# Kernel tuning notes

Measured on AMD Instinct MI355X. Metric: run time of the kernel, lower is better.

Reference implementation:

```python
import jax, jax.numpy as jnp
import numpy as np

B, C, T = 64, 64, 1000   # batch, EEG channels (input_dim), timesteps
H = 512                   # hidden_dim
L = 3                     # num_layers
NC = 5                    # num_classes


def setup_inputs() -> dict:
    key = jax.random.key(0)
    ks = jax.random.split(key, 9)
    s_in = 1.0 / np.sqrt(H)  # torch LSTM init scale
    x = jax.random.normal(ks[0], (B, C, T), dtype=jnp.float32)
    W_ih0 = jax.random.uniform(ks[1], (4 * H, C), jnp.float32, -s_in, s_in)
    W_ih_rest = jax.random.uniform(ks[2], (L - 1, 4 * H, H), jnp.float32, -s_in, s_in)
    W_hh = jax.random.uniform(ks[3], (L, 4 * H, H), jnp.float32, -s_in, s_in)
    b_ih = jax.random.uniform(ks[4], (L, 4 * H), jnp.float32, -s_in, s_in)
    b_hh = jax.random.uniform(ks[5], (L, 4 * H), jnp.float32, -s_in, s_in)
    W_fc = jax.random.uniform(ks[6], (NC, H), jnp.float32, -s_in, s_in)
    b_fc = jax.random.uniform(ks[7], (NC,), jnp.float32, -s_in, s_in)
    return {"x": x, "W_ih0": W_ih0, "W_ih_rest": W_ih_rest, "W_hh": W_hh,
            "b_ih": b_ih, "b_hh": b_hh, "W_fc": W_fc, "b_fc": b_fc}


def _lstm_layer(x_tbc, W_ih, W_hh, b):
    """x_tbc: [T, B, in]. Returns (h_seq [T,B,H], h_T [B,H]). Gate order i,f,g,o (PyTorch)."""
    # Precompute input projections for all timesteps: [T, B, 4H]
    xg = jnp.einsum('tbi,gi->tbg', x_tbc, W_ih) + b

    def step(carry, xg_t):
        h, c = carry
        gates = xg_t + h @ W_hh.T  # [B, 4H]
        i, f, g, o = jnp.split(gates, 4, axis=-1)
        i, f, o = jax.nn.sigmoid(i), jax.nn.sigmoid(f), jax.nn.sigmoid(o)
        g = jnp.tanh(g)
        c = f * c + i * g
        h = o * jnp.tanh(c)
        return (h, c), h

    Bn = x_tbc.shape[1]
    h0 = jnp.zeros((Bn, H), x_tbc.dtype)
    (hT, _), h_seq = jax.lax.scan(step, (h0, h0), xg)
    return h_seq, hT


def reference(x, W_ih0, W_ih_rest, W_hh, b_ih, b_hh, W_fc, b_fc):
    # input_type='signal': [B, C, T] -> batch_first [B, T, C]; scan over time-major [T, B, C]
    seq = jnp.transpose(x, (2, 0, 1))  # [T, B, C]
    hT = None
    for l in range(L):
        W_ih = W_ih0 if l == 0 else W_ih_rest[l - 1]
        seq, hT = _lstm_layer(seq, W_ih, W_hh[l], b_ih[l] + b_hh[l])
    # dropout=0 (inference): identity
    return hT @ W_fc.T + b_fc  # [B, NC]
```

## Files before the change

kernel.cpp:

```cpp
#include <hip/hip_runtime.h>
#include <cstdint>

#define TB 64
#define TC 64
#define TT 1000
#define TH 512
#define NCLS 5
#define NTHR 512
#define STEPS 1002

#define H0_OFF 0
#define H1_OFF 8192
#define H2_OFF 16384
#define X_OFF  24576
#define SC_OFF 32768
#define SC_W   864
#define LDS_FLOATS (SC_OFF + 8 * SC_W)
#define LDS_BYTES  (LDS_FLOATS * 4)

__device__ __forceinline__ float sigf(float x) { return 1.0f / (1.0f + expf(-x)); }

__device__ __forceinline__ void pin4(float4& v) {
  asm volatile("" : "+v"(v.x), "+v"(v.y), "+v"(v.z), "+v"(v.w));
}

__device__ __forceinline__ void group_barrier(int* gb, int s) {
  __syncthreads();
  if (threadIdx.x == 0) {
    const int target = s + 1;
    int a = __hip_atomic_fetch_add(gb + 0, 1, __ATOMIC_RELAXED, __HIP_MEMORY_SCOPE_AGENT);
    if (a == 64 * target - 1)
      __hip_atomic_fetch_add(gb + 8, 1, __ATOMIC_RELAXED, __HIP_MEMORY_SCOPE_AGENT);
    while (__hip_atomic_load(gb + 8, __ATOMIC_RELAXED, __HIP_MEMORY_SCOPE_AGENT) < target)
      __builtin_amdgcn_s_sleep(1);
    unsigned xcc;
    asm volatile("s_getreg_b32 %0, hwreg(HW_REG_XCC_ID)" : "=s"(xcc));
    int expected = s;
    if (__hip_atomic_compare_exchange_strong(gb + 32 + (xcc & 7), &expected, target,
            __ATOMIC_RELAXED, __ATOMIC_RELAXED, __HIP_MEMORY_SCOPE_AGENT)) {
      __threadfence();
    }
    int d = __hip_atomic_fetch_add(gb + 16, 1, __ATOMIC_RELAXED, __HIP_MEMORY_SCOPE_AGENT);
    if (d == 64 * target - 1)
      __hip_atomic_fetch_add(gb + 24, 1, __ATOMIC_RELAXED, __HIP_MEMORY_SCOPE_AGENT);
    while (__hip_atomic_load(gb + 24, __ATOMIC_RELAXED, __HIP_MEMORY_SCOPE_AGENT) < target)
      __builtin_amdgcn_s_sleep(1);
  }
  __syncthreads();
}

__device__ __forceinline__ void dot4(float& acc, const float4 a, const float4 b) {
  acc = fmaf(a.x, b.x, acc); acc = fmaf(a.y, b.y, acc);
  acc = fmaf(a.z, b.z, acc); acc = fmaf(a.w, b.w, acc);
}

__device__ __forceinline__ void gload_lds16_cg(const char* gsrc_lane, char* lds_base) {
  __builtin_amdgcn_global_load_lds(
      (const __attribute__((address_space(1))) unsigned int*)gsrc_lane,
      (__attribute__((address_space(3))) unsigned int*)lds_base, 16, 0, 0x11);
}

__global__ __launch_bounds__(NTHR) __attribute__((amdgpu_waves_per_eu(2, 2)))
void lstm_pipe(
    const float* __restrict__ x, const float* __restrict__ Wih0,
    const float* __restrict__ WihR, const float* __restrict__ Whh,
    const float* __restrict__ bih, const float* __restrict__ bhh,
    float* __restrict__ hbuf, int* __restrict__ bar)
{
  __shared__ float lds[LDS_FLOATS];
  const int tid = threadIdx.x;
  const int blk = blockIdx.x;
  const int grp = blk >> 6, slot = blk & 63;
  const int b_base = grp * 16;
  const int kk = tid >> 5;
  const int rt = tid & 31;
  const int g  = rt & 3;
  const int cl = rt >> 2;
  const int cell = slot * 8 + cl;
  const int row  = g * TH + cell;
  const int wv = tid >> 6;
  const int lane = tid & 63;

  int* gb = bar + grp * 64;

  float4 wx, wh0[8], w1a[8], w1b[8], w2a[8], w2b[8];
  wx = *(const float4*)(Wih0 + (size_t)row * TC + 4 * kk);
  pin4(wx);
  {
    const float* p0 = Whh  + (size_t)row * TH + 32 * kk;
    const float* p1 = WihR + (size_t)row * TH + 32 * kk;
    const float* p2 = Whh  + (size_t)(2048 + row) * TH + 32 * kk;
    const float* p3 = WihR + (size_t)(2048 + row) * TH + 32 * kk;
    const float* p4 = Whh  + (size_t)(4096 + row) * TH + 32 * kk;
#pragma unroll
    for (int i = 0; i < 8; ++i) {
      wh0[i] = *(const float4*)(p0 + 4 * i); pin4(wh0[i]);
      w1a[i] = *(const float4*)(p1 + 4 * i); pin4(w1a[i]);
      w1b[i] = *(const float4*)(p2 + 4 * i); pin4(w1b[i]);
      w2a[i] = *(const float4*)(p3 + 4 * i); pin4(w2a[i]);
      w2b[i] = *(const float4*)(p4 + 4 * i); pin4(w2b[i]);
    }
  }

  const int rl = tid >> 6;
  const int rc = (tid & 63) >> 3;
  const int rb = tid & 7;
  const int rcell = slot * 8 + rc;
  float4 bias_r = make_float4(0.f, 0.f, 0.f, 0.f);
  if (tid < 192) {
    bias_r.x = bih[rl * 2048 + rcell]        + bhh[rl * 2048 + rcell];
    bias_r.y = bih[rl * 2048 +  512 + rcell] + bhh[rl * 2048 +  512 + rcell];
    bias_r.z = bih[rl * 2048 + 1024 + rcell] + bhh[rl * 2048 + 1024 + rcell];
    bias_r.w = bih[rl * 2048 + 1536 + rcell] + bhh[rl * 2048 + 1536 + rcell];
  }
  float cst0 = 0.f, cst1 = 0.f;

  for (int s = 0; s < STEPS; ++s) {
    {
      const bool v0 = (s >= 1 && s <= 1000);
      const bool v1 = (s >= 2);
      const bool v2 = (s >= 3);
      const bool vc = ((s & 7) == 0 && s <= 999);
      if (v0) {
        const char* gp = (const char*)(hbuf + ((size_t)(0 + ((s - 1) & 1)) * TB + b_base) * TH);
        char* lb = (char*)lds + H0_OFF * 4;
#pragma unroll
        for (int i = 0; i < 4; ++i) {
          int off = wv * 4096 + i * 1024;
          gload_lds16_cg(gp + off + lane * 16, lb + off);
        }
      }
      if (v1) {
        const char* gp = (const char*)(hbuf + ((size_t)(2 + ((s - 2) & 1)) * TB + b_base) * TH);
        char* lb = (char*)lds + H1_OFF * 4;
#pragma unroll
        for (int i = 0; i < 4; ++i) {
          int off = wv * 4096 + i * 1024;
          gload_lds16_cg(gp + off + lane * 16, lb + off);
        }
      }
      if (v2) {
        const char* gp = (const char*)(hbuf + ((size_t)(4 + ((s - 3) & 1)) * TB + b_base) * TH);
        char* lb = (char*)lds + H2_OFF * 4;
#pragma unroll
        for (int i = 0; i < 4; ++i) {
          int off = wv * 4096 + i * 1024;
          gload_lds16_cg(gp + off + lane * 16, lb + off);
        }
      }
      if (vc) {
        const int e0 = tid, e1 = tid + NTHR;
        const float* q0 = x + (size_t)(b_base + (e0 >> 6)) * (TC * TT) + (size_t)(e0 & 63) * TT + s;
        const float* q1 = x + (size_t)(b_base + (e1 >> 6)) * (TC * TT) + (size_t)(e1 & 63) * TT + s;
        float4 xa0 = *(const float4*)(q0), xa1 = *(const float4*)(q0 + 4);
        float4 xb0 = *(const float4*)(q1), xb1 = *(const float4*)(q1 + 4);
        float* d0 = lds + X_OFF + (e0 >> 6) * 64 + (e0 & 63);
        float* d1 = lds + X_OFF + (e1 >> 6) * 64 + (e1 & 63);
        d0[0 * 1024] = xa0.x; d0[1 * 1024] = xa0.y; d0[2 * 1024] = xa0.z; d0[3 * 1024] = xa0.w;
        d0[4 * 1024] = xa1.x; d0[5 * 1024] = xa1.y; d0[6 * 1024] = xa1.z; d0[7 * 1024] = xa1.w;
        d1[0 * 1024] = xb0.x; d1[1 * 1024] = xb0.y; d1[2 * 1024] = xb0.z; d1[3 * 1024] = xb0.w;
        d1[4 * 1024] = xb1.x; d1[5 * 1024] = xb1.y; d1[6 * 1024] = xb1.z; d1[7 * 1024] = xb1.w;
      }
    }
    __syncthreads();

#pragma unroll
    for (int p = 0; p < 2; ++p) {
      float a0[8], a1[8], a2[8];
#pragma unroll
      for (int b = 0; b < 8; ++b) { a0[b] = 0.f; a1[b] = 0.f; a2[b] = 0.f; }
#pragma unroll
      for (int b = 0; b < 8; ++b) {
        const int bb = p * 8 + b;
        if (s <= 999) {
          float4 xf = *(const float4*)(lds + X_OFF + (s & 7) * 1024 + bb * 64 + 4 * kk);
          dot4(a0[b], wx, xf);
        }
        if (s >= 1 && s <= 1000) {
          const float* hb = lds + H0_OFF + bb * TH + 32 * kk;
#pragma unroll
          for (int c4 = 0; c4 < 2; ++c4) {
            float4 f0 = *(const float4*)(hb + 16 * c4 + 0);
            float4 f1 = *(const float4*)(hb + 16 * c4 + 4);
            float4 f2 = *(const float4*)(hb + 16 * c4 + 8);
            float4 f3 = *(const float4*)(hb + 16 * c4 + 12);
            if (s <= 999) {
              dot4(a0[b], wh0[4 * c4 + 0], f0); dot4(a0[b], wh0[4 * c4 + 1], f1);
              dot4(a0[b], wh0[4 * c4 + 2], f2); dot4(a0[b], wh0[4 * c4 + 3], f3);
            }
            dot4(a1[b], w1a[4 * c4 + 0], f0); dot4(a1[b], w1a[4 * c4 + 1], f1);
            dot4(a1[b], w1a[4 * c4 + 2], f2); dot4(a1[b], w1a[4 * c4 + 3], f3);
          }
        }
        if (s >= 2) {
          const float* hb = lds + H1_OFF + bb * TH + 32 * kk;
#pragma unroll
          for (int c4 = 0; c4 < 2; ++c4) {
            float4 f0 = *(const float4*)(hb + 16 * c4 + 0);
            float4 f1 = *(const float4*)(hb + 16 * c4 + 4);
            float4 f2 = *(const float4*)(hb + 16 * c4 + 8);
            float4 f3 = *(const float4*)(hb + 16 * c4 + 12);
            if (s <= 1000) {
              dot4(a1[b], w1b[4 * c4 + 0], f0); dot4(a1[b], w1b[4 * c4 + 1], f1);
              dot4(a1[b], w1b[4 * c4 + 2], f2); dot4(a1[b], w1b[4 * c4 + 3], f3);
            }
            dot4(a2[b], w2a[4 * c4 + 0], f0); dot4(a2[b], w2a[4 * c4 + 1], f1);
            dot4(a2[b], w2a[4 * c4 + 2], f2); dot4(a2[b], w2a[4 * c4 + 3], f3);
          }
        }
        if (s >= 3) {
          const float* hb = lds + H2_OFF + bb * TH + 32 * kk;
#pragma unroll
          for (int c4 = 0; c4 < 2; ++c4) {
            float4 f0 = *(const float4*)(hb + 16 * c4 + 0);
            float4 f1 = *(const float4*)(hb + 16 * c4 + 4);
            float4 f2 = *(const float4*)(hb + 16 * c4 + 8);
            float4 f3 = *(const float4*)(hb + 16 * c4 + 12);
            dot4(a2[b], w2b[4 * c4 + 0], f0); dot4(a2[b], w2b[4 * c4 + 1], f1);
            dot4(a2[b], w2b[4 * c4 + 2], f2); dot4(a2[b], w2b[4 * c4 + 3], f3);
          }
        }
      }
#pragma unroll
      for (int b = 0; b < 8; ++b) {
        a0[b] += __shfl_xor(a0[b], 32, 64);
        a1[b] += __shfl_xor(a1[b], 32, 64);
        a2[b] += __shfl_xor(a2[b], 32, 64);
      }
      if ((tid & 32) == 0) {
        float* sb = lds + SC_OFF + wv * SC_W + cl * 36 + g;
#pragma unroll
        for (int b = 0; b < 8; ++b) {
          sb[4 * b]       = a0[b];
          sb[288 + 4 * b] = a1[b];
          sb[576 + 4 * b] = a2[b];
        }
      }
      __syncthreads();
      if (tid < 192) {
        const int tl = s - rl;
        if (tl >= 0 && tl < TT) {
          float sx = 0.f, sy = 0.f, sz = 0.f, sw = 0.f;
          const float* sb = lds + SC_OFF + rl * 288 + rc * 36 + 4 * rb;
#pragma unroll
          for (int w8 = 0; w8 < 8; ++w8) {
            float4 v = *(const float4*)(sb + w8 * SC_W);
            sx += v.x; sy += v.y; sz += v.z; sw += v.w;
          }
          float ii = sigf(sx + bias_r.x);
          float ff = sigf(sy + bias_r.y);
          float gg = tanhf(sz + bias_r.z);
          float oo = sigf(sw + bias_r.w);
          float cprev = p ? cst1 : cst0;
          float cc = (tl == 0) ? ii * gg : fmaf(ff, cprev, ii * gg);
          if (p) cst1 = cc; else cst0 = cc;
          float hh = oo * tanhf(cc);
          hbuf[((size_t)(rl * 2 + (tl & 1)) * TB + b_base + p * 8 + rb) * TH + rcell] = hh;
        }
      }
      __syncthreads();
    }
    group_barrier(gb, s);
  }
}

__global__ void fc_kernel(const float* __restrict__ hbuf, const float* __restrict__ Wfc,
                          const float* __restrict__ bfc, float* __restrict__ out) {
  int bb = blockIdx.x, lane = threadIdx.x;
  const float* h = hbuf + ((size_t)5 * TB + bb) * TH;
  for (int n = 0; n < NCLS; ++n) {
    float s = 0.f;
    for (int k = lane; k < TH; k += 64) s = fmaf(h[k], Wfc[n * TH + k], s);
    for (int off = 32; off > 0; off >>= 1) s += __shfl_down(s, off, 64);
    if (lane == 0) out[bb * NCLS + n] = s + bfc[n];
  }
}

extern "C" void kernel_launch(void* const* d_in, const int* in_sizes, int n_in,
                              void* d_out, int out_size, void* d_ws, size_t ws_size,
                              hipStream_t stream) {
  const float* x    = (const float*)d_in[0];
  const float* Wih0 = (const float*)d_in[1];
  const float* WihR = (const float*)d_in[2];
  const float* Whh  = (const float*)d_in[3];
  const float* bih  = (const float*)d_in[4];
  const float* bhh  = (const float*)d_in[5];
  const float* Wfc  = (const float*)d_in[6];
  const float* bfc  = (const float*)d_in[7];
  float* out = (float*)d_out;

  char* ws = (char*)d_ws;
  int*   bar  = (int*)ws;
  float* hbuf = (float*)(ws + 1024);

  hipMemsetAsync(bar, 0, 1024, stream);
  lstm_pipe<<<256, NTHR, 0, stream>>>(x, Wih0, WihR, Whh, bih, bhh, hbuf, bar);
  fc_kernel<<<TB, 64, 0, stream>>>(hbuf, Wfc, bfc, out);
}
```

Baseline: 18.64 ms.

## Replace two-phase grid barrier with hierarchical per-XCD barrier

The grid barrier used by every timestep becomes hierarchical. At startup each block counts how many blocks share its XCD and how many XCDs are occupied. Each step, blocks increment a per-XCD counter, and only the last block on each XCD fences and bumps a global counter. All blocks then spin on a single release flag. This cuts contended global atomics and removes one full spin phase per step. The risk is memory-ordering correctness, since only one fence is issued per XCD.

```diff
diff --git a/kernel.cpp b/kernel.cpp
--- a/kernel.cpp
+++ b/kernel.cpp
@@ -24,26 +24,19 @@
   asm volatile("" : "+v"(v.x), "+v"(v.y), "+v"(v.z), "+v"(v.w));
 }
 
-__device__ __forceinline__ void group_barrier(int* gb, int s) {
+__device__ __forceinline__ void group_barrier(int* gb, int s, unsigned xcc,
+                                              int occ_mine, int nxcd) {
   __syncthreads();
   if (threadIdx.x == 0) {
-    const int target = s + 1;
-    int a = __hip_atomic_fetch_add(gb + 0, 1, __ATOMIC_RELAXED, __HIP_MEMORY_SCOPE_AGENT);
-    if (a == 64 * target - 1)
-      __hip_atomic_fetch_add(gb + 8, 1, __ATOMIC_RELAXED, __HIP_MEMORY_SCOPE_AGENT);
-    while (__hip_atomic_load(gb + 8, __ATOMIC_RELAXED, __HIP_MEMORY_SCOPE_AGENT) < target)
-      __builtin_amdgcn_s_sleep(1);
-    unsigned xcc;
-    asm volatile("s_getreg_b32 %0, hwreg(HW_REG_XCC_ID)" : "=s"(xcc));
-    int expected = s;
-    if (__hip_atomic_compare_exchange_strong(gb + 32 + (xcc & 7), &expected, target,
-            __ATOMIC_RELAXED, __ATOMIC_RELAXED, __HIP_MEMORY_SCOPE_AGENT)) {
+    const int t = s + 1;
+    int a = __hip_atomic_fetch_add(gb + 16 + xcc, 1, __ATOMIC_RELAXED, __HIP_MEMORY_SCOPE_AGENT);
+    if (a == occ_mine * t - 1) {
       __threadfence();
-    }
-    int d = __hip_atomic_fetch_add(gb + 16, 1, __ATOMIC_RELAXED, __HIP_MEMORY_SCOPE_AGENT);
-    if (d == 64 * target - 1)
-      __hip_atomic_fetch_add(gb + 24, 1, __ATOMIC_RELAXED, __HIP_MEMORY_SCOPE_AGENT);
-    while (__hip_atomic_load(gb + 24, __ATOMIC_RELAXED, __HIP_MEMORY_SCOPE_AGENT) < target)
+      int d = __hip_atomic_fetch_add(gb + 32, 1, __ATOMIC_RELAXED, __HIP_MEMORY_SCOPE_AGENT);
+      if (d == nxcd * t - 1)
+        __hip_atomic_fetch_add(gb + 40, 1, __ATOMIC_RELAXED, __HIP_MEMORY_SCOPE_AGENT);
+    }
+    while (__hip_atomic_load(gb + 40, __ATOMIC_RELAXED, __HIP_MEMORY_SCOPE_AGENT) < t)
       __builtin_amdgcn_s_sleep(1);
   }
   __syncthreads();
@@ -115,6 +108,27 @@
   }
   float cst0 = 0.f, cst1 = 0.f;
 
+  unsigned xcc = 0;
+  int occ_mine = 0, nxcd = 0;
+  if (tid == 0) {
+    unsigned xr;
+    asm volatile("s_getreg_b32 %0, hwreg(HW_REG_XCC_ID)" : "=s"(xr));
+    xcc = xr & 7;
+    __hip_atomic_fetch_add(gb + 8 + xcc, 1, __ATOMIC_RELAXED, __HIP_MEMORY_SCOPE_AGENT);
+    int a = __hip_atomic_fetch_add(gb + 0, 1, __ATOMIC_RELAXED, __HIP_MEMORY_SCOPE_AGENT);
+    if (a == 63)
+      __hip_atomic_fetch_add(gb + 4, 1, __ATOMIC_RELAXED, __HIP_MEMORY_SCOPE_AGENT);
+    while (__hip_atomic_load(gb + 4, __ATOMIC_RELAXED, __HIP_MEMORY_SCOPE_AGENT) < 1)
+      __builtin_amdgcn_s_sleep(1);
+#pragma unroll
+    for (int i = 0; i < 8; ++i) {
+      int o = __hip_atomic_load(gb + 8 + i, __ATOMIC_RELAXED, __HIP_MEMORY_SCOPE_AGENT);
+      if (i == (int)xcc) occ_mine = o;
+      if (o > 0) ++nxcd;
+    }
+  }
+  __syncthreads();
+
   for (int s = 0; s < STEPS; ++s) {
     {
       const bool v0 = (s >= 1 && s <= 1000);
@@ -260,7 +274,7 @@
       }
       __syncthreads();
     }
-    group_barrier(gb, s);
+    group_barrier(gb, s, xcc, occ_mine, nxcd);
   }
 }
 
```

Result: faster. 17.16 ms (-7.9%).
